# Performance work log

Measured on AMD Instinct MI355X. Metric: run time of the kernel, lower is better.

Reference implementation:

```python
import jax, jax.numpy as jnp
import numpy as np

B, T, H, L = 32, 256, 1024, 2
FORGET_BIAS = 1.0


def setup_inputs() -> dict:
    key = jax.random.key(0)
    k1, k2, k3, k4 = jax.random.split(key, 4)
    x = jax.random.normal(k1, (B, T, H), dtype=jnp.float32)
    lengths = jax.random.randint(k2, (B,), 1, T + 1, dtype=jnp.int32)
    Wx = jax.random.normal(k3, (L, H, 4 * H), dtype=jnp.float32) * 0.02
    Wh = jax.random.normal(k4, (L, H, 4 * H), dtype=jnp.float32) * 0.02
    b = jnp.zeros((L, 4 * H), dtype=jnp.float32)
    return {"x": x, "lengths": lengths, "Wx": Wx, "Wh": Wh, "b": b}


def _lstm_layer(x, lengths, Wx, Wh, b):
    """One TF-style LSTM layer over time with dynamic_rnn length masking.
    Gate order (i, j, f, o), forget_bias added to f. Returns (outputs, (h_T, c_T))."""
    Bb, Tt, _ = x.shape
    Hh = Wh.shape[0]
    # precompute input projections for all steps: [B, T, 4H]
    xproj = jnp.einsum('bti,ig->btg', x, Wx) + b

    def step(carry, inp):
        h, c = carry
        xt, t = inp  # xt: [B, 4H], t: scalar step index
        z = xt + h @ Wh  # [B, 4H]
        i, j, f, o = jnp.split(z, 4, axis=-1)
        c_new = jax.nn.sigmoid(f + FORGET_BIAS) * c + jax.nn.sigmoid(i) * jnp.tanh(j)
        h_new = jax.nn.sigmoid(o) * jnp.tanh(c_new)
        mask = (t < lengths)[:, None]  # [B,1]
        h2 = jnp.where(mask, h_new, h)
        c2 = jnp.where(mask, c_new, c)
        out = jnp.where(mask, h_new, 0.0)  # dynamic_rnn zeros outputs past length
        return (h2, c2), out

    init = (jnp.zeros((Bb, Hh), x.dtype), jnp.zeros((Bb, Hh), x.dtype))
    (hT, cT), outs = jax.lax.scan(step, init, (xproj.transpose(1, 0, 2), jnp.arange(Tt)))
    return outs.transpose(1, 0, 2), (hT, cT)


def reference(x, lengths, Wx, Wh, b):
    inp = x
    hs, cs = [], []
    for l in range(L):  # fixed small layer stack
        inp, (hT, cT) = _lstm_layer(inp, lengths, Wx[l], Wh[l], b[l])
        hs.append(hT)
        cs.append(cT)
    # rnnout: [B,T,H]; hidden: per-layer final (c,h) like TF LSTMStateTuple
    return inp, jnp.stack(cs), jnp.stack(hs)
```

## Files before the change

kernel.cpp:

```cpp
#include <hip/hip_runtime.h>

typedef unsigned short u16;
typedef unsigned int u32;
typedef unsigned long long u64;
typedef __attribute__((ext_vector_type(8))) short short8;
typedef __attribute__((ext_vector_type(4))) float f32x4;
typedef __attribute__((ext_vector_type(4))) u32 u32x4;
typedef __attribute__((ext_vector_type(2))) u32 u32x2;

#define RN_ 8388608
#define MFMA16(a, b, c) __builtin_amdgcn_mfma_f32_16x16x32_bf16(a, b, c, 0, 0, 0)

__device__ __forceinline__ u16 f2bf(float f) {
  union { float f; u32 u; } v; v.f = f;
  u32 r = v.u + 0x7fffu + ((v.u >> 16) & 1u);
  return (u16)(r >> 16);
}
__device__ __forceinline__ float bf2f(u16 h) {
  union { u32 u; float f; } v; v.u = ((u32)h) << 16;
  return v.f;
}
__device__ __forceinline__ u32 pk2(float a, float b) {
  return (u32)f2bf(a) | ((u32)f2bf(b) << 16);
}
__device__ __forceinline__ int permcol(int R) {
  return (R & 3) * 1024 + ((R >> 5) << 3) + ((R >> 2) & 7);
}
__device__ __forceinline__ float sigm(float x) { return 1.f / (1.f + __expf(-x)); }
__device__ __forceinline__ float tanh_(float x) {
  float e = __expf(2.f * x);
  return 1.f - 2.f / (e + 1.f);
}

__global__ __launch_bounds__(256) void transpose_convert(
    const float* __restrict__ Wx, const float* __restrict__ Wh,
    u16* __restrict__ WxT1, u16* __restrict__ WxT2,
    u16* __restrict__ WhT1, u16* __restrict__ WhT2) {
  __shared__ float lds[64][65];
  const int bid = blockIdx.x, tid = threadIdx.x;
  const int sel = bid >> 10;
  const int tile = bid & 1023;
  const int kt = tile & 15, rt = tile >> 4;
  const float* src;
  u16* dst;
  if (sel == 0)      { src = Wx;                       dst = WxT1; }
  else if (sel == 1) { src = Wx + (size_t)1024 * 4096; dst = WxT2; }
  else if (sel == 2) { src = Wh;                       dst = WhT1; }
  else               { src = Wh + (size_t)1024 * 4096; dst = WhT2; }
#pragma unroll
  for (int ii = 0; ii < 16; ++ii) {
    int idx = ii * 256 + tid;
    int r = idx >> 6, c = idx & 63;
    int run = c >> 3, u = c & 7;
    int blkLoc = run >> 2, gate = run & 3;
    int g = gate * 1024 + (rt * 2 + blkLoc) * 8 + u;
    lds[r][blkLoc * 32 + u * 4 + gate] = src[(size_t)(kt * 64 + r) * 4096 + g];
  }
  __syncthreads();
#pragma unroll
  for (int ii = 0; ii < 16; ++ii) {
    int idx = ii * 256 + tid;
    int rw = idx >> 6, cw = idx & 63;
    dst[(size_t)(rt * 64 + rw) * 1024 + kt * 64 + cw] = f2bf(lds[cw][rw]);
  }
}

template <int IS2>
__device__ void gemm_grp(char* smem, int gb,
    const float* __restrict__ Af32, const u16* __restrict__ Ahp,
    const u16* __restrict__ Bt, const float* __restrict__ bias,
    u16* __restrict__ Cring, const int* flags, int* gdone) {
  u16* As = (u16*)smem;
  u16* Bs = (u16*)(smem + 16384);
  const int tid = threadIdx.x;
  const int lane = tid & 63, w = tid >> 6;
  const int wm = w >> 1, wn = w & 1;
  const int l15 = lane & 15, lq = lane >> 4;
  const int srow = tid >> 2, qd = tid & 3;
  const u32 rsw = (u32)((l15 & 7) << 4);

  for (int c = 0; c < 16; ++c) {
    if (w == 0) {
      const int thrA = IS2 ? 16 * (c + 1) : 16 * c - 48;
      const int thrB = 16 * c - 48;
      while (1) {
        bool ok = true;
        if (lane < 16) {
          u32x4 fv;
          const u32x4* fp = (const u32x4*)flags + lane;
          asm volatile("global_load_dwordx4 %0, %1, off sc0 sc1"
                       : "=v"(fv) : "v"(fp) : "memory");
          asm volatile("s_waitcnt vmcnt(0)" ::: "memory");
          __builtin_amdgcn_sched_barrier(0);
          ok = (int)fv[0] >= thrA && (int)fv[1] >= thrA &&
               (int)fv[2] >= thrA && (int)fv[3] >= thrA;
        } else if (IS2 && lane < 32) {
          u32x4 fv;
          const u32x4* fp = (const u32x4*)(flags + 64) + (lane - 16);
          asm volatile("global_load_dwordx4 %0, %1, off sc0 sc1"
                       : "=v"(fv) : "v"(fp) : "memory");
          asm volatile("s_waitcnt vmcnt(0)" ::: "memory");
          __builtin_amdgcn_sched_barrier(0);
          ok = (int)fv[0] >= thrB && (int)fv[1] >= thrB &&
               (int)fv[2] >= thrB && (int)fv[3] >= thrB;
        }
        if (__all(ok)) break;
        __builtin_amdgcn_s_sleep(8);
      }
    }
    __syncthreads();

    for (int e = 0; e < 2; ++e) {
      const int ti = gb * 2 + e;
      const int mg = ti >> 5, ng = ti & 31;

      f32x4 acc[4][4];
#pragma unroll
      for (int i = 0; i < 4; ++i)
#pragma unroll
        for (int j = 0; j < 4; ++j) acc[i][j] = (f32x4){0.f, 0.f, 0.f, 0.f};

      for (int kt = 0; kt < 16; ++kt) {
        u32x4 aw[2][2], bv[2][2];
#pragma unroll
        for (int rr = 0; rr < 2; ++rr) {
          int row = rr * 64 + srow;
          const u32x4* bp = (const u32x4*)(Bt + (size_t)(ng * 128 + row) * 1024 + kt * 64 + qd * 16);
          bv[rr][0] = bp[0]; bv[rr][1] = bp[1];
          int rg = 512 * c + mg * 128 + row;
          if (IS2) {
            int tq = rg >> 5, b2 = rg & 31;
            int p = kt * 8 + qd * 2;
            const char* ap = (const char*)Ahp + (size_t)tq * 65536 +
                             (size_t)(p * 32 + b2) * 16;
            asm volatile("global_load_dwordx4 %0, %1, off sc0 sc1"
                         : "=v"(aw[rr][0]) : "v"(ap) : "memory");
            asm volatile("global_load_dwordx4 %0, %1, off sc0 sc1"
                         : "=v"(aw[rr][1]) : "v"(ap + 512) : "memory");
          } else {
            const f32x4* ap = (const f32x4*)(Af32 +
                ((size_t)(rg & 31) * 256 + (rg >> 5)) * 1024 + kt * 64 + qd * 16);
            f32x4 a0 = ap[0], a1 = ap[1], a2 = ap[2], a3 = ap[3];
            aw[rr][0][0] = pk2(a0[0], a0[1]); aw[rr][0][1] = pk2(a0[2], a0[3]);
            aw[rr][0][2] = pk2(a1[0], a1[1]); aw[rr][0][3] = pk2(a1[2], a1[3]);
            aw[rr][1][0] = pk2(a2[0], a2[1]); aw[rr][1][1] = pk2(a2[2], a2[3]);
            aw[rr][1][2] = pk2(a3[0], a3[1]); aw[rr][1][3] = pk2(a3[2], a3[3]);
          }
        }
        __syncthreads();
        if (IS2) {
          asm volatile("s_waitcnt vmcnt(0)" ::: "memory");
          __builtin_amdgcn_sched_barrier(0);
        }
#pragma unroll
        for (int rr = 0; rr < 2; ++rr) {
          int row = rr * 64 + srow;
          u32 sw = (u32)((row & 7) << 4);
          int base = row * 128 + qd * 32;
          *(u32x4*)((char*)As + ((base) ^ sw)) = aw[rr][0];
          *(u32x4*)((char*)As + ((base + 16) ^ sw)) = aw[rr][1];
          *(u32x4*)((char*)Bs + ((base) ^ sw)) = bv[rr][0];
          *(u32x4*)((char*)Bs + ((base + 16) ^ sw)) = bv[rr][1];
        }
        __syncthreads();
#pragma unroll
        for (int k2 = 0; k2 < 2; ++k2) {
          short8 af[4], bf[4];
#pragma unroll
          for (int f = 0; f < 4; ++f) {
            af[f] = *(const short8*)((const char*)As +
                     (((wm * 64 + f * 16 + l15) * 128 + k2 * 64 + lq * 16) ^ rsw));
            bf[f] = *(const short8*)((const char*)Bs +
                     (((wn * 64 + f * 16 + l15) * 128 + k2 * 64 + lq * 16) ^ rsw));
          }
#pragma unroll
          for (int fi = 0; fi < 4; ++fi)
#pragma unroll
            for (int fj = 0; fj < 4; ++fj)
              acc[fi][fj] = MFMA16(af[fi], bf[fj], acc[fi][fj]);
        }
      }
#pragma unroll
      for (int fj = 0; fj < 4; ++fj) {
        int gc = ng * 128 + wn * 64 + fj * 16 + l15;
        float bvv = bias[permcol(gc)];
#pragma unroll
        for (int fi = 0; fi < 4; ++fi) {
          int rr0 = (c & 3) * 512 + mg * 128 + wm * 64 + fi * 16 + lq * 4;
#pragma unroll
          for (int r = 0; r < 4; ++r) {
            u32 vv = (u32)f2bf(acc[fi][fj][r] + bvv);
            const u16* cp = Cring + (size_t)(rr0 + r) * 4096 + gc;
            asm volatile("global_store_short %0, %1, off sc0 sc1"
                         :: "v"(cp), "v"(vv) : "memory");
          }
        }
      }
      __syncthreads();
    }
    asm volatile("s_waitcnt vmcnt(0)" ::: "memory");
    if (tid == 0)
      __hip_atomic_fetch_add(gdone + c, 1, __ATOMIC_RELAXED, __HIP_MEMORY_SCOPE_AGENT);
  }
}

template <int L>
__device__ void scan_grp(char* smem, int nb,
    const u16* __restrict__ xpring, const u16* __restrict__ Wt,
    const int* __restrict__ lengths, u64* hpub,
    int* flags_self, const int* gdone,
    float* __restrict__ outp, float* __restrict__ csf, float* __restrict__ hsf) {
  f32x4* partv = (f32x4*)smem;
  u16* h_stage = (u16*)(smem + 32768);
  float* out_stage = (float*)(smem + 33792);
  const int tid = threadIdx.x;
  const int lane = tid & 63, w = tid >> 6;
  const int l15 = lane & 15, q = lane >> 4;
  const int b = (w & 1) * 16 + l15;
  const int u0 = (w >> 1) * 4 + q;
  const int len = lengths[b];

  short8 afr[4][8];
#pragma unroll
  for (int tt = 0; tt < 4; ++tt)
#pragma unroll
    for (int ks = 0; ks < 8; ++ks)
      afr[tt][ks] = *(const short8*)(Wt + (size_t)(nb * 64 + tt * 16 + l15) * 1024 +
                                     w * 256 + ks * 32 + q * 8);

  f32x4 acc[4][2];
#pragma unroll
  for (int tt = 0; tt < 4; ++tt)
#pragma unroll
    for (int bc = 0; bc < 2; ++bc) acc[tt][bc] = (f32x4){0.f, 0.f, 0.f, 0.f};
  float c0 = 0.f, h0 = 0.f, c1 = 0.f, h1 = 0.f;

  for (int t = 0; t < 256; ++t) {
    if ((t & 15) == 0) {
      if (w == 0) {
        const int cidx = t >> 4;
        while (1) {
          bool ok = true;
          if (lane == 0) {
            u32 cd;
            asm volatile("global_load_dword %0, %1, off sc0 sc1"
                         : "=v"(cd) : "v"(gdone + cidx) : "memory");
            asm volatile("s_waitcnt vmcnt(0)" ::: "memory");
            __builtin_amdgcn_sched_barrier(0);
            ok = (int)cd >= 64;
          }
          if (__all(ok)) break;
          __builtin_amdgcn_s_sleep(2);
        }
      }
      __syncthreads();
    }

    const u16* xa = xpring + ((size_t)((t >> 4) & 3) * 512 + (t & 15) * 32 + b) * 4096 +
                    nb * 64 + u0 * 4;
    u32x2 xpv0, xpv1;
    asm volatile("global_load_dwordx2 %0, %1, off sc0 sc1"
                 : "=v"(xpv0) : "v"(xa) : "memory");
    asm volatile("global_load_dwordx2 %0, %1, off sc0 sc1"
                 : "=v"(xpv1) : "v"(xa + 32) : "memory");

    if (t > 0) {
      const char* hp = (const char*)hpub + (size_t)(t - 1) * 65536;
      short8 bfv[16];
      while (1) {
#pragma unroll
        for (int i = 0; i < 16; ++i) {
          const int ks = i >> 1, bc = i & 1;
          const char* p = hp + (((w * 32 + ks * 4 + q) * 32 + bc * 16 + l15) << 4);
          asm volatile("global_load_dwordx4 %0, %1, off sc0 sc1"
                       : "=v"(bfv[i]) : "v"(p) : "memory");
        }
        asm volatile("s_waitcnt vmcnt(0)" ::: "memory");
        __builtin_amdgcn_sched_barrier(0);
        bool ok = true;
#pragma unroll
        for (int i = 0; i < 16; ++i) {
          u32x4 vv = __builtin_bit_cast(u32x4, bfv[i]);
          ok = ok && (vv[0] != 0xFFFFFFFFu) && (vv[1] != 0xFFFFFFFFu) &&
               (vv[2] != 0xFFFFFFFFu) && (vv[3] != 0xFFFFFFFFu);
        }
        if (__all(ok)) break;
        __builtin_amdgcn_s_sleep(1);
      }
      __builtin_amdgcn_sched_barrier(0);
#pragma unroll
      for (int i = 0; i < 16; ++i) {
        const int ks = i >> 1, bc = i & 1;
        acc[0][bc] = MFMA16(afr[0][ks], bfv[i], acc[0][bc]);
        acc[1][bc] = MFMA16(afr[1][ks], bfv[i], acc[1][bc]);
        acc[2][bc] = MFMA16(afr[2][ks], bfv[i], acc[2][bc]);
        acc[3][bc] = MFMA16(afr[3][ks], bfv[i], acc[3][bc]);
      }
    } else {
      asm volatile("s_waitcnt vmcnt(0)" ::: "memory");
      __builtin_amdgcn_sched_barrier(0);
    }

#pragma unroll
    for (int tt = 0; tt < 4; ++tt)
#pragma unroll
      for (int bc = 0; bc < 2; ++bc) {
        partv[(w * 8 + tt * 2 + bc) * 64 + lane] = acc[tt][bc];
        acc[tt][bc] = (f32x4){0.f, 0.f, 0.f, 0.f};
      }
    __syncthreads();
    f32x4 s0 = (f32x4){0.f, 0.f, 0.f, 0.f};
    f32x4 s1 = (f32x4){0.f, 0.f, 0.f, 0.f};
#pragma unroll
    for (int w2 = 0; w2 < 4; ++w2) {
      s0 += partv[(w2 * 8 + w) * 64 + lane];
      s1 += partv[(w2 * 8 + 4 + w) * 64 + lane];
    }

    bool mk = t < len;
    {
      float zi = s0[0] + bf2f((u16)(xpv0[0] & 0xffffu));
      float zj = s0[1] + bf2f((u16)(xpv0[0] >> 16));
      float zf = s0[2] + bf2f((u16)(xpv0[1] & 0xffffu)) + 1.f;
      float zo = s0[3] + bf2f((u16)(xpv0[1] >> 16));
      float cn = sigm(zf) * c0 + sigm(zi) * tanh_(zj);
      float hn = sigm(zo) * tanh_(cn);
      c0 = mk ? cn : c0;
      h0 = mk ? hn : h0;
      float ov = mk ? hn : 0.f;
      h_stage[b * 16 + u0] = f2bf(ov);
      if (L) out_stage[b * 16 + u0] = ov;
    }
    {
      float zi = s1[0] + bf2f((u16)(xpv1[0] & 0xffffu));
      float zj = s1[1] + bf2f((u16)(xpv1[0] >> 16));
      float zf = s1[2] + bf2f((u16)(xpv1[1] & 0xffffu)) + 1.f;
      float zo = s1[3] + bf2f((u16)(xpv1[1] >> 16));
      float cn = sigm(zf) * c1 + sigm(zi) * tanh_(zj);
      float hn = sigm(zo) * tanh_(cn);
      c1 = mk ? cn : c1;
      h1 = mk ? hn : h1;
      float ov = mk ? hn : 0.f;
      h_stage[b * 16 + u0 + 8] = f2bf(ov);
      if (L) out_stage[b * 16 + u0 + 8] = ov;
    }
    __syncthreads();

    if (tid < 64) {
      int p = tid >> 5, bb = tid & 31;
      u32x4 pv = *(const u32x4*)((const char*)h_stage + bb * 32 + p * 16);
      char* hd = (char*)hpub + (size_t)t * 65536 +
                 (size_t)((nb * 2 + p) * 32 + bb) * 16;
      asm volatile("global_store_dwordx4 %0, %1, off sc0 sc1"
                   :: "v"(hd), "v"(pv) : "memory");
    }
    if (((t + 1) & 15) == 0 && w == 0) {
      asm volatile("s_waitcnt vmcnt(0)" ::: "memory");
      if (tid == 0)
        __hip_atomic_store(flags_self + nb, t + 1, __ATOMIC_RELAXED,
                           __HIP_MEMORY_SCOPE_AGENT);
    }
    if (L && tid < 128) {
      int bb = tid >> 2, part = tid & 3;
      f32x4 ov = *(const f32x4*)(out_stage + bb * 16 + part * 4);
      *(f32x4*)(outp + ((size_t)bb * 256 + t) * 1024 + nb * 16 + part * 4) = ov;
    }
  }
  csf[L * 32768 + b * 1024 + nb * 16 + u0] = c0;
  csf[L * 32768 + b * 1024 + nb * 16 + u0 + 8] = c1;
  hsf[L * 32768 + b * 1024 + nb * 16 + u0] = h0;
  hsf[L * 32768 + b * 1024 + nb * 16 + u0 + 8] = h1;
}

__global__ __launch_bounds__(256, 1) void lstm_pipe(
    const float* __restrict__ x, const int* __restrict__ lengths,
    const float* __restrict__ bias,
    const u16* __restrict__ WxT1, const u16* __restrict__ WxT2,
    const u16* __restrict__ WhT1, const u16* __restrict__ WhT2,
    u16* xp1ring, u16* xp2ring,
    u64* hpub1, u64* hpub2, int* flags, float* outp) {
  __shared__ __align__(16) char smem[35840];
  int* g1done = flags + 128;
  int* g2done = flags + 144;
  const int bid = blockIdx.x;
  float* csf = outp + RN_;
  float* hsf = csf + 65536;
  if (bid < 64)
    gemm_grp<0>(smem, bid, x, nullptr, WxT1, bias, xp1ring, flags, g1done);
  else if (bid < 128)
    scan_grp<0>(smem, bid - 64, xp1ring, WhT1, lengths, hpub1, flags, g1done,
                outp, csf, hsf);
  else if (bid < 192)
    gemm_grp<1>(smem, bid - 128, nullptr, (const u16*)hpub1, WxT2, bias + 4096,
                xp2ring, flags, g2done);
  else
    scan_grp<1>(smem, bid - 192, xp2ring, WhT2, lengths, hpub2, flags + 64, g2done,
                outp, csf, hsf);
}

#define WS_WXT1 0u
#define WS_WXT2 (8u << 20)
#define WS_WHT1 (16u << 20)
#define WS_WHT2 (24u << 20)
#define WS_XP1 (32u << 20)
#define WS_XP2 (48u << 20)
#define WS_HPUB1 (64u << 20)
#define WS_HPUB2 (80u << 20)
#define WS_FLAGS (96u << 20)

extern "C" void kernel_launch(void* const* d_in, const int* in_sizes, int n_in,
                              void* d_out, int out_size, void* d_ws, size_t ws_size,
                              hipStream_t stream) {
  const float* x = (const float*)d_in[0];
  const int* lengths = (const int*)d_in[1];
  const float* Wx = (const float*)d_in[2];
  const float* Wh = (const float*)d_in[3];
  const float* bias = (const float*)d_in[4];
  float* outp = (float*)d_out;

  if (ws_size < (size_t)WS_FLAGS + 4096) return;

  char* ws = (char*)d_ws;
  u16* WxT1 = (u16*)(ws + WS_WXT1);
  u16* WxT2 = (u16*)(ws + WS_WXT2);
  u16* WhT1 = (u16*)(ws + WS_WHT1);
  u16* WhT2 = (u16*)(ws + WS_WHT2);
  u16* xp1ring = (u16*)(ws + WS_XP1);
  u16* xp2ring = (u16*)(ws + WS_XP2);
  u64* hpub1 = (u64*)(ws + WS_HPUB1);
  u64* hpub2 = (u64*)(ws + WS_HPUB2);
  int* flags = (int*)(ws + WS_FLAGS);

  hipMemsetAsync(flags, 0, 2048, stream);
  hipMemsetAsync(hpub1, 0xFF, 32u << 20, stream);
  transpose_convert<<<4096, 256, 0, stream>>>(Wx, Wh, WxT1, WxT2, WhT1, WhT2);
  lstm_pipe<<<256, 256, 0, stream>>>(x, lengths, bias, WxT1, WxT2, WhT1, WhT2,
                                     xp1ring, xp2ring, hpub1, hpub2, flags, outp);
}
```

Before: 1.232 ms.

## Halve GEMM chunk granularity and poll only unready h fragments in scan

The input-projection GEMM blocks now handle one 128x128 tile per chunk over 32 chunks of 8 timesteps instead of two tiles over 16 chunks of 16 timesteps. Flag thresholds, ring indexing and scan publish cadence are all adjusted to match. This should shorten pipeline fill and let the recurrent scan start sooner. The scan's spin-wait for the previous hidden state now reissues loads only for fragments that still read as sentinel values, which cuts redundant global traffic while polling. The risks are more frequent flag synchronization, a larger gdone array (g2done moved offset), and per-fragment __all checks adding overhead on the critical path.

```diff
diff --git a/kernel.cpp b/kernel.cpp
--- a/kernel.cpp
+++ b/kernel.cpp
@@ -77,12 +77,13 @@
   const int wm = w >> 1, wn = w & 1;
   const int l15 = lane & 15, lq = lane >> 4;
   const int srow = tid >> 2, qd = tid & 3;
+  const int mg = gb >> 5, ng = gb & 31;
   const u32 rsw = (u32)((l15 & 7) << 4);
 
-  for (int c = 0; c < 16; ++c) {
+  for (int c = 0; c < 32; ++c) {
     if (w == 0) {
-      const int thrA = IS2 ? 16 * (c + 1) : 16 * c - 48;
-      const int thrB = 16 * c - 48;
+      const int thrA = IS2 ? 8 * (c + 1) : 8 * c - 24;
+      const int thrB = 8 * c - 24;
       while (1) {
         bool ok = true;
         if (lane < 16) {
@@ -110,99 +111,114 @@
     }
     __syncthreads();
 
-    for (int e = 0; e < 2; ++e) {
-      const int ti = gb * 2 + e;
-      const int mg = ti >> 5, ng = ti & 31;
-
-      f32x4 acc[4][4];
-#pragma unroll
-      for (int i = 0; i < 4; ++i)
-#pragma unroll
-        for (int j = 0; j < 4; ++j) acc[i][j] = (f32x4){0.f, 0.f, 0.f, 0.f};
-
-      for (int kt = 0; kt < 16; ++kt) {
-        u32x4 aw[2][2], bv[2][2];
-#pragma unroll
-        for (int rr = 0; rr < 2; ++rr) {
-          int row = rr * 64 + srow;
-          const u32x4* bp = (const u32x4*)(Bt + (size_t)(ng * 128 + row) * 1024 + kt * 64 + qd * 16);
-          bv[rr][0] = bp[0]; bv[rr][1] = bp[1];
-          int rg = 512 * c + mg * 128 + row;
-          if (IS2) {
-            int tq = rg >> 5, b2 = rg & 31;
-            int p = kt * 8 + qd * 2;
-            const char* ap = (const char*)Ahp + (size_t)tq * 65536 +
-                             (size_t)(p * 32 + b2) * 16;
-            asm volatile("global_load_dwordx4 %0, %1, off sc0 sc1"
-                         : "=v"(aw[rr][0]) : "v"(ap) : "memory");
-            asm volatile("global_load_dwordx4 %0, %1, off sc0 sc1"
-                         : "=v"(aw[rr][1]) : "v"(ap + 512) : "memory");
-          } else {
-            const f32x4* ap = (const f32x4*)(Af32 +
-                ((size_t)(rg & 31) * 256 + (rg >> 5)) * 1024 + kt * 64 + qd * 16);
-            f32x4 a0 = ap[0], a1 = ap[1], a2 = ap[2], a3 = ap[3];
-            aw[rr][0][0] = pk2(a0[0], a0[1]); aw[rr][0][1] = pk2(a0[2], a0[3]);
-            aw[rr][0][2] = pk2(a1[0], a1[1]); aw[rr][0][3] = pk2(a1[2], a1[3]);
-            aw[rr][1][0] = pk2(a2[0], a2[1]); aw[rr][1][1] = pk2(a2[2], a2[3]);
-            aw[rr][1][2] = pk2(a3[0], a3[1]); aw[rr][1][3] = pk2(a3[2], a3[3]);
-          }
-        }
-        __syncthreads();
+    f32x4 acc[4][4];
+#pragma unroll
+    for (int i = 0; i < 4; ++i)
+#pragma unroll
+      for (int j = 0; j < 4; ++j) acc[i][j] = (f32x4){0.f, 0.f, 0.f, 0.f};
+
+    for (int kt = 0; kt < 16; ++kt) {
+      u32x4 aw[2][2], bv[2][2];
+#pragma unroll
+      for (int rr = 0; rr < 2; ++rr) {
+        int row = rr * 64 + srow;
+        const u32x4* bp = (const u32x4*)(Bt + (size_t)(ng * 128 + row) * 1024 + kt * 64 + qd * 16);
+        bv[rr][0] = bp[0]; bv[rr][1] = bp[1];
+        int rg = 256 * c + mg * 128 + row;
         if (IS2) {
-          asm volatile("s_waitcnt vmcnt(0)" ::: "memory");
-          __builtin_amdgcn_sched_barrier(0);
-        }
-#pragma unroll
-        for (int rr = 0; rr < 2; ++rr) {
-          int row = rr * 64 + srow;
-          u32 sw = (u32)((row & 7) << 4);
-          int base = row * 128 + qd * 32;
-          *(u32x4*)((char*)As + ((base) ^ sw)) = aw[rr][0];
-          *(u32x4*)((char*)As + ((base + 16) ^ sw)) = aw[rr][1];
-          *(u32x4*)((char*)Bs + ((base) ^ sw)) = bv[rr][0];
-          *(u32x4*)((char*)Bs + ((base + 16) ^ sw)) = bv[rr][1];
-        }
-        __syncthreads();
-#pragma unroll
-        for (int k2 = 0; k2 < 2; ++k2) {
-          short8 af[4], bf[4];
-#pragma unroll
-          for (int f = 0; f < 4; ++f) {
-            af[f] = *(const short8*)((const char*)As +
-                     (((wm * 64 + f * 16 + l15) * 128 + k2 * 64 + lq * 16) ^ rsw));
-            bf[f] = *(const short8*)((const char*)Bs +
-                     (((wn * 64 + f * 16 + l15) * 128 + k2 * 64 + lq * 16) ^ rsw));
-          }
-#pragma unroll
-          for (int fi = 0; fi < 4; ++fi)
-#pragma unroll
-            for (int fj = 0; fj < 4; ++fj)
-              acc[fi][fj] = MFMA16(af[fi], bf[fj], acc[fi][fj]);
-        }
-      }
-#pragma unroll
-      for (int fj = 0; fj < 4; ++fj) {
-        int gc = ng * 128 + wn * 64 + fj * 16 + l15;
-        float bvv = bias[permcol(gc)];
-#pragma unroll
-        for (int fi = 0; fi < 4; ++fi) {
-          int rr0 = (c & 3) * 512 + mg * 128 + wm * 64 + fi * 16 + lq * 4;
-#pragma unroll
-          for (int r = 0; r < 4; ++r) {
-            u32 vv = (u32)f2bf(acc[fi][fj][r] + bvv);
-            const u16* cp = Cring + (size_t)(rr0 + r) * 4096 + gc;
-            asm volatile("global_store_short %0, %1, off sc0 sc1"
-                         :: "v"(cp), "v"(vv) : "memory");
-          }
+          int tq = rg >> 5, b2 = rg & 31;
+          int p = kt * 8 + qd * 2;
+          const char* ap = (const char*)Ahp + (size_t)tq * 65536 +
+                           (size_t)(p * 32 + b2) * 16;
+          asm volatile("global_load_dwordx4 %0, %1, off sc0 sc1"
+                       : "=v"(aw[rr][0]) : "v"(ap) : "memory");
+          asm volatile("global_load_dwordx4 %0, %1, off sc0 sc1"
+                       : "=v"(aw[rr][1]) : "v"(ap + 512) : "memory");
+        } else {
+          const f32x4* ap = (const f32x4*)(Af32 +
+              ((size_t)(rg & 31) * 256 + (rg >> 5)) * 1024 + kt * 64 + qd * 16);
+          f32x4 a0 = ap[0], a1 = ap[1], a2 = ap[2], a3 = ap[3];
+          aw[rr][0][0] = pk2(a0[0], a0[1]); aw[rr][0][1] = pk2(a0[2], a0[3]);
+          aw[rr][0][2] = pk2(a1[0], a1[1]); aw[rr][0][3] = pk2(a1[2], a1[3]);
+          aw[rr][1][0] = pk2(a2[0], a2[1]); aw[rr][1][1] = pk2(a2[2], a2[3]);
+          aw[rr][1][2] = pk2(a3[0], a3[1]); aw[rr][1][3] = pk2(a3[2], a3[3]);
         }
       }
       __syncthreads();
+      if (IS2) {
+        asm volatile("s_waitcnt vmcnt(0)" ::: "memory");
+        __builtin_amdgcn_sched_barrier(0);
+      }
+#pragma unroll
+      for (int rr = 0; rr < 2; ++rr) {
+        int row = rr * 64 + srow;
+        u32 sw = (u32)((row & 7) << 4);
+        int base = row * 128 + qd * 32;
+        *(u32x4*)((char*)As + ((base) ^ sw)) = aw[rr][0];
+        *(u32x4*)((char*)As + ((base + 16) ^ sw)) = aw[rr][1];
+        *(u32x4*)((char*)Bs + ((base) ^ sw)) = bv[rr][0];
+        *(u32x4*)((char*)Bs + ((base + 16) ^ sw)) = bv[rr][1];
+      }
+      __syncthreads();
+#pragma unroll
+      for (int k2 = 0; k2 < 2; ++k2) {
+        short8 af[4], bf[4];
+#pragma unroll
+        for (int f = 0; f < 4; ++f) {
+          af[f] = *(const short8*)((const char*)As +
+                   (((wm * 64 + f * 16 + l15) * 128 + k2 * 64 + lq * 16) ^ rsw));
+          bf[f] = *(const short8*)((const char*)Bs +
+                   (((wn * 64 + f * 16 + l15) * 128 + k2 * 64 + lq * 16) ^ rsw));
+        }
+#pragma unroll
+        for (int fi = 0; fi < 4; ++fi)
+#pragma unroll
+          for (int fj = 0; fj < 4; ++fj)
+            acc[fi][fj] = MFMA16(af[fi], bf[fj], acc[fi][fj]);
+      }
+    }
+#pragma unroll
+    for (int fj = 0; fj < 4; ++fj) {
+      int gc = ng * 128 + wn * 64 + fj * 16 + l15;
+      float bvv = bias[permcol(gc)];
+#pragma unroll
+      for (int fi = 0; fi < 4; ++fi) {
+        int rr0 = (c & 3) * 256 + mg * 128 + wm * 64 + fi * 16 + lq * 4;
+#pragma unroll
+        for (int r = 0; r < 4; ++r) {
+          u32 vv = (u32)f2bf(acc[fi][fj][r] + bvv);
+          const u16* cp = Cring + (size_t)(rr0 + r) * 4096 + gc;
+          asm volatile("global_store_short %0, %1, off sc0 sc1"
+                       :: "v"(cp), "v"(vv) : "memory");
+        }
+      }
     }
     asm volatile("s_waitcnt vmcnt(0)" ::: "memory");
+    __syncthreads();
     if (tid == 0)
       __hip_atomic_fetch_add(gdone + c, 1, __ATOMIC_RELAXED, __HIP_MEMORY_SCOPE_AGENT);
   }
 }
+
+#define ISSUE_FRAG(B, i_) do { \
+  const int g_ = (i_) >> 2, j_ = (i_) & 3; \
+  if (j_ == 0) asm volatile("global_load_dwordx4 %0, %1, off sc0 sc1" \
+                            : "=v"(B[i_]) : "v"(pa[g_]) : "memory"); \
+  else if (j_ == 1) asm volatile("global_load_dwordx4 %0, %1, off offset:256 sc0 sc1" \
+                                 : "=v"(B[i_]) : "v"(pa[g_]) : "memory"); \
+  else if (j_ == 2) asm volatile("global_load_dwordx4 %0, %1, off offset:2048 sc0 sc1" \
+                                 : "=v"(B[i_]) : "v"(pa[g_]) : "memory"); \
+  else asm volatile("global_load_dwordx4 %0, %1, off offset:2304 sc0 sc1" \
+                    : "=v"(B[i_]) : "v"(pa[g_]) : "memory"); \
+} while (0)
+#define DRAIN0() do { asm volatile("s_waitcnt vmcnt(0)" ::: "memory"); \
+  __builtin_amdgcn_sched_barrier(0); } while (0)
+#define MFALL(B) do { _Pragma("unroll") for (int i_ = 0; i_ < 16; ++i_) { \
+  const int ks_ = i_ >> 1, bc_ = i_ & 1; \
+  acc[0][bc_] = MFMA16(afr[0][ks_], B[i_], acc[0][bc_]); \
+  acc[1][bc_] = MFMA16(afr[1][ks_], B[i_], acc[1][bc_]); \
+  acc[2][bc_] = MFMA16(afr[2][ks_], B[i_], acc[2][bc_]); \
+  acc[3][bc_] = MFMA16(afr[3][ks_], B[i_], acc[3][bc_]); } } while (0)
 
 template <int L>
 __device__ void scan_grp(char* smem, int nb,
@@ -235,10 +251,12 @@
     for (int bc = 0; bc < 2; ++bc) acc[tt][bc] = (f32x4){0.f, 0.f, 0.f, 0.f};
   float c0 = 0.f, h0 = 0.f, c1 = 0.f, h1 = 0.f;
 
+  const int lane_base = (w * 32 + q) * 512 + l15 * 16;
+
   for (int t = 0; t < 256; ++t) {
-    if ((t & 15) == 0) {
+    if ((t & 7) == 0) {
       if (w == 0) {
-        const int cidx = t >> 4;
+        const int cidx = t >> 3;
         while (1) {
           bool ok = true;
           if (lane == 0) {
@@ -256,7 +274,7 @@
       __syncthreads();
     }
 
-    const u16* xa = xpring + ((size_t)((t >> 4) & 3) * 512 + (t & 15) * 32 + b) * 4096 +
+    const u16* xa = xpring + ((size_t)((t >> 3) & 3) * 256 + (t & 7) * 32 + b) * 4096 +
                     nb * 64 + u0 * 4;
     u32x2 xpv0, xpv1;
     asm volatile("global_load_dwordx2 %0, %1, off sc0 sc1"
@@ -265,40 +283,36 @@
                  : "=v"(xpv1) : "v"(xa + 32) : "memory");
 
     if (t > 0) {
-      const char* hp = (const char*)hpub + (size_t)(t - 1) * 65536;
+      const char* hp = (const char*)hpub + (size_t)(t - 1) * 65536 + lane_base;
+      const char* pa[4];
+#pragma unroll
+      for (int g = 0; g < 4; ++g) pa[g] = hp + g * 4096;
       short8 bfv[16];
+#pragma unroll
+      for (int i = 0; i < 16; ++i) ISSUE_FRAG(bfv, i);
+      u32 done = 0;
       while (1) {
-#pragma unroll
-        for (int i = 0; i < 16; ++i) {
-          const int ks = i >> 1, bc = i & 1;
-          const char* p = hp + (((w * 32 + ks * 4 + q) * 32 + bc * 16 + l15) << 4);
-          asm volatile("global_load_dwordx4 %0, %1, off sc0 sc1"
-                       : "=v"(bfv[i]) : "v"(p) : "memory");
-        }
-        asm volatile("s_waitcnt vmcnt(0)" ::: "memory");
-        __builtin_amdgcn_sched_barrier(0);
-        bool ok = true;
-#pragma unroll
-        for (int i = 0; i < 16; ++i) {
-          u32x4 vv = __builtin_bit_cast(u32x4, bfv[i]);
-          ok = ok && (vv[0] != 0xFFFFFFFFu) && (vv[1] != 0xFFFFFFFFu) &&
-               (vv[2] != 0xFFFFFFFFu) && (vv[3] != 0xFFFFFFFFu);
-        }
-        if (__all(ok)) break;
-        __builtin_amdgcn_s_sleep(1);
+        DRAIN0();
+        {
+#pragma unroll
+          for (int i = 0; i < 16; ++i) {
+            if (!(done & (1u << i))) {
+              u32x4 vv = __builtin_bit_cast(u32x4, bfv[i]);
+              bool ok = vv[0] != 0xFFFFFFFFu && vv[1] != 0xFFFFFFFFu &&
+                        vv[2] != 0xFFFFFFFFu && vv[3] != 0xFFFFFFFFu;
+              if (__all(ok)) done |= (1u << i);
+            }
+          }
+        }
+        if (done == 0xFFFFu) break;
+#pragma unroll
+        for (int i = 0; i < 16; ++i)
+          if (!(done & (1u << i))) ISSUE_FRAG(bfv, i);
       }
       __builtin_amdgcn_sched_barrier(0);
-#pragma unroll
-      for (int i = 0; i < 16; ++i) {
-        const int ks = i >> 1, bc = i & 1;
-        acc[0][bc] = MFMA16(afr[0][ks], bfv[i], acc[0][bc]);
-        acc[1][bc] = MFMA16(afr[1][ks], bfv[i], acc[1][bc]);
-        acc[2][bc] = MFMA16(afr[2][ks], bfv[i], acc[2][bc]);
-        acc[3][bc] = MFMA16(afr[3][ks], bfv[i], acc[3][bc]);
-      }
+      MFALL(bfv);
     } else {
-      asm volatile("s_waitcnt vmcnt(0)" ::: "memory");
-      __builtin_amdgcn_sched_barrier(0);
+      DRAIN0();
     }
 
 #pragma unroll
@@ -354,7 +368,7 @@
       asm volatile("global_store_dwordx4 %0, %1, off sc0 sc1"
                    :: "v"(hd), "v"(pv) : "memory");
     }
-    if (((t + 1) & 15) == 0 && w == 0) {
+    if (((t + 1) & 7) == 0 && w == 0) {
       asm volatile("s_waitcnt vmcnt(0)" ::: "memory");
       if (tid == 0)
         __hip_atomic_store(flags_self + nb, t + 1, __ATOMIC_RELAXED,
@@ -381,7 +395,7 @@
     u64* hpub1, u64* hpub2, int* flags, float* outp) {
   __shared__ __align__(16) char smem[35840];
   int* g1done = flags + 128;
-  int* g2done = flags + 144;
+  int* g2done = flags + 160;
   const int bid = blockIdx.x;
   float* csf = outp + RN_;
   float* hsf = csf + 65536;
```

After: 1.255 ms. No clear change (+1.9%).
